# Performance work log

Hardware: AMD Instinct MI355X
Metric: run time of the kernel (lower is better)

The kernel has to match this reference:

```python
import jax, jax.numpy as jnp
import numpy as np

ALPHA = 0.2          # LeakyReLU negative slope
BN_EPS = 1e-5
NEG_INF = -9e15


def setup_inputs() -> dict:
    key = jax.random.key(0)
    k1, k2, k3, k4 = jax.random.split(key, 4)
    B, N, Fin, Fout = 4, 4096, 64, 64
    h = jax.random.normal(k1, (B, N, Fin), dtype=jnp.float32)
    adj = jax.random.randint(k2, (N, N), 0, 2, dtype=jnp.int32)
    # xavier_uniform with gain 1.414
    gain = 1.414
    bW = gain * np.sqrt(6.0 / (Fin + Fout))
    W = jax.random.uniform(k3, (Fin, Fout), dtype=jnp.float32, minval=-bW, maxval=bW)
    ba = gain * np.sqrt(6.0 / (2 * Fout + 1))
    a = jax.random.uniform(k4, (2 * Fout, 1), dtype=jnp.float32, minval=-ba, maxval=ba)
    gamma = jnp.ones((N,), dtype=jnp.float32)
    beta = jnp.zeros((N,), dtype=jnp.float32)
    return {"h": h, "adj": adj, "W": W, "a": a, "gamma": gamma, "beta": beta}


def reference(h, adj, W, a, gamma, beta):
    # h: [B,N,Fin], adj: [N,N], W: [Fin,Fout], a: [2*Fout,1]
    N = adj.shape[0]
    Fout = W.shape[1]
    dk = jnp.asarray(N, h.dtype) ** 0.5
    Wh = jnp.einsum('bnf,fo->bno', h, W)                # [B,N,Fout]
    Wh1 = Wh @ a[:Fout]                                 # [B,N,1]
    Wh2 = Wh @ a[Fout:]                                 # [B,N,1]
    e = (Wh1 + jnp.swapaxes(Wh2, 1, 2)) / dk            # [B,N,N] broadcast add
    e = jax.nn.leaky_relu(e, negative_slope=ALPHA)
    scores = jnp.where(adj[None] > 0, e, NEG_INF)
    attention = jax.nn.softmax(scores, axis=2)          # dropout is identity at inference
    h_prime = jnp.einsum('bij,bjo->bio', attention, Wh) # [B,N,Fout]
    # BatchNorm1d(N): channel axis is the node axis, normalize over (B, Fout)
    mean = h_prime.mean(axis=(0, 2), keepdims=True)
    var = h_prime.var(axis=(0, 2), keepdims=True)
    h_prime = gamma[None, :, None] * (h_prime - mean) * jax.lax.rsqrt(var + BN_EPS) + beta[None, :, None]
    out = h_prime + h                                   # in==out -> res_net is None
    return jax.nn.elu(out)                              # concat=True
```

## Files before the change

### kernel.cpp

```cpp
#include <hip/hip_runtime.h>
#include <hip/hip_fp16.h>
#include <math.h>

#define NN 4096
#define SCL 0.022542110013890054f
#define LOG2E 1.4426950408889634f

typedef __attribute__((ext_vector_type(8))) _Float16 f16x8;
typedef __attribute__((ext_vector_type(2))) _Float16 f16x2;
typedef __attribute__((ext_vector_type(4))) float f32x4;
typedef __attribute__((ext_vector_type(4))) short s16x4;

__device__ __forceinline__ float exp2_fast(float x) {
  float r; asm("v_exp_f32 %0, %1" : "=v"(r) : "v"(x)); return r;
}
__device__ __forceinline__ unsigned short h16(float x) {
  _Float16 h = (_Float16)x; return *(unsigned short*)&h;
}

__global__ __launch_bounds__(256)
void k_prep(const float* __restrict__ h, const float* __restrict__ W,
            const float* __restrict__ a, const int* __restrict__ adj,
            unsigned short* __restrict__ WhTf, unsigned* __restrict__ Ei1,
            unsigned* __restrict__ Ei2, unsigned* __restrict__ Ej1,
            unsigned* __restrict__ Ej2, unsigned* __restrict__ bits) {
  __shared__ float sW[4096];
  __shared__ unsigned short T[64][8];
  const int t = threadIdx.x;
  const int bi = blockIdx.x;
  const int r3 = bi % 3, q3 = bi / 3;
  if (r3 == 0) {
    const int w = t >> 6, lane = t & 63;
    const int r = q3 * 4 + w;
    const int kq = lane >> 1, hi = lane & 1;
#pragma unroll
    for (int half = 0; half < 2; ++half) {
      const int* __restrict__ src = adj + ((size_t)r << 12) + half * 2048;
      int v[32];
#pragma unroll
      for (int k = 0; k < 32; ++k) v[k] = src[k * 64 + lane];
      unsigned myw = 0;
#pragma unroll
      for (int k = 0; k < 32; ++k) {
        unsigned long long m = __ballot(v[k] != 0);
        unsigned lohi = hi ? (unsigned)(m >> 32) : (unsigned)m;
        myw = (kq == k) ? lohi : myw;
      }
      bits[((size_t)r << 7) + half * 64 + lane] = myw;
    }
    return;
  }
#pragma unroll
  for (int i = 0; i < 16; ++i) sW[i * 256 + t] = W[i * 256 + t];
  __syncthreads();
  const int wv = t >> 6, lane = t & 63;
  const float a1 = a[lane], a2 = a[64 + lane];
  const int row0 = (q3 * 2 + (r3 - 1)) * 8;
  const int q0 = row0 + wv * 2;
  float w1v[2], w2v[2];
  for (int r = 0; r < 2; ++r) {
    const int row = q0 + r;
    const float* hr = h + (size_t)row * 64;
    float acc = 0.f;
#pragma unroll
    for (int k = 0; k < 64; ++k) acc = fmaf(hr[k], sW[k * 64 + lane], acc);
    T[lane][wv * 2 + r] = h16(acc);
    float r1 = acc * a1, r2 = acc * a2;
#pragma unroll
    for (int sft = 32; sft; sft >>= 1) { r1 += __shfl_xor(r1, sft); r2 += __shfl_xor(r2, sft); }
    w1v[r] = r1 * SCL; w2v[r] = r2 * SCL;
  }
  if (lane == 0) {
#pragma unroll
    for (int r = 0; r < 2; ++r) {
      unsigned u1 = h16(exp2_fast(w1v[r]));
      unsigned u2 = h16(exp2_fast(0.2f * w1v[r]));
      Ei1[q0 + r] = u1 | (u1 << 16);
      Ei2[q0 + r] = u2 | (u2 << 16);
    }
    Ej1[q0 >> 1] = (unsigned)h16(exp2_fast(w2v[0])) |
                   ((unsigned)h16(exp2_fast(w2v[1])) << 16);
    Ej2[q0 >> 1] = (unsigned)h16(exp2_fast(0.2f * w2v[0])) |
                   ((unsigned)h16(exp2_fast(0.2f * w2v[1])) << 16);
  }
  __syncthreads();
  const int f = t >> 2, jp4 = t & 3;
  const int b = row0 >> 12, n0 = row0 & 4095;
  const int g32 = n0 >> 5, rgq = (n0 >> 3) & 3;
  unsigned v = *(unsigned*)&T[f][jp4 * 2];
  unsigned short* dst = WhTf +
      ((((size_t)(b * 4 + (f >> 4)) << 7) + g32) << 9) +
      ((rgq * 16 + (f & 15)) << 3) + jp4 * 2;
  *(unsigned*)dst = v;
}

__global__ __launch_bounds__(512, 2)
void k_gat(const unsigned* __restrict__ bits,
           const unsigned short* __restrict__ WhTf,
           const unsigned* __restrict__ Ei1, const unsigned* __restrict__ Ei2,
           const unsigned* __restrict__ Ej1, const unsigned* __restrict__ Ej2,
           unsigned short* __restrict__ Pp, float* __restrict__ lsp) {
  __shared__ unsigned mlds[256][17];

  const int t = threadIdx.x;
  const int w = t >> 6, lane = t & 63;
  const int jp = lane & 15, rg = lane >> 4;
  const int bid = blockIdx.x;
  const int c = bid >> 6;
  const int b = (bid >> 4) & 3;
  const int i0b = (bid & 15) * 256;
  const int i0 = i0b + w * 32;
  const int g0 = c * 16;

#pragma unroll
  for (int pass = 0; pass < 8; ++pass) {
    const int row = pass * 32 + (t >> 4);
    mlds[row][t & 15] = bits[((size_t)(i0b + row) << 7) + g0 + (t & 15)];
  }

  unsigned ei1u[2], ei2u[2];
#pragma unroll
  for (int il = 0; il < 2; ++il) {
    ei1u[il] = Ei1[b * NN + i0 + il * 16 + jp];
    ei2u[il] = Ei2[b * NN + i0 + il * 16 + jp];
  }
  const unsigned short* __restrict__ abase =
      WhTf + (((size_t)(b * 4) << 7) + g0) * 512 + lane * 8;
  const unsigned* __restrict__ ej1b = Ej1 + (b << 11) + (g0 << 4) + (rg << 2);
  const unsigned* __restrict__ ej2b = Ej2 + (b << 11) + (g0 << 4) + (rg << 2);

  f32x4 acc[2][4];
  f32x4 accd[2];
#pragma unroll
  for (int il = 0; il < 2; ++il) {
    accd[il] = (f32x4){0.f, 0.f, 0.f, 0.f};
#pragma unroll
    for (int ft = 0; ft < 4; ++ft) acc[il][ft] = (f32x4){0.f, 0.f, 0.f, 0.f};
  }
  f16x8 ones;
#pragma unroll
  for (int e = 0; e < 8; ++e) ones[e] = (_Float16)1.0f;

  __syncthreads();

#pragma unroll 2
  for (int jt = 0; jt < 16; ++jt) {
    const f16x8 af0 = *(const f16x8*)(abase + (0 * 128 + jt) * 512);
    const f16x8 af1 = *(const f16x8*)(abase + (1 * 128 + jt) * 512);
    const f16x8 af2 = *(const f16x8*)(abase + (2 * 128 + jt) * 512);
    const f16x8 af3 = *(const f16x8*)(abase + (3 * 128 + jt) * 512);
    const uint4 e1p = *(const uint4*)(ej1b + jt * 16);
    const uint4 e2p = *(const uint4*)(ej2b + jt * 16);
    const unsigned e1a[4] = {e1p.x, e1p.y, e1p.z, e1p.w};
    const unsigned e2a[4] = {e2p.x, e2p.y, e2p.z, e2p.w};

    f16x8 pf[2];
#pragma unroll
    for (int il = 0; il < 2; ++il) {
      const unsigned mb = mlds[w * 32 + il * 16 + jp][jt] >> (rg * 8);
      const f16x2 x1 = *(const f16x2*)&ei1u[il];
      const f16x2 x2 = *(const f16x2*)&ei2u[il];
      unsigned pw[4];
#pragma unroll
      for (int p4 = 0; p4 < 4; ++p4) {
        f16x2 c1 = x1 * (*(const f16x2*)&e1a[p4]);
        f16x2 c2 = x2 * (*(const f16x2*)&e2a[p4]);
        f16x2 mx = __builtin_elementwise_max(c1, c2);
        unsigned mexp = (((mb >> (2 * p4)) & 1u) ? 0xFFFFu : 0u) |
                        (((mb >> (2 * p4 + 1)) & 1u) ? 0xFFFF0000u : 0u);
        pw[p4] = (*(unsigned*)&mx) & mexp;
      }
      pf[il] = *(f16x8*)pw;
    }
#pragma unroll
    for (int il = 0; il < 2; ++il) {
      accd[il] = __builtin_amdgcn_mfma_f32_16x16x32_f16(ones, pf[il], accd[il], 0, 0, 0);
      acc[il][0] = __builtin_amdgcn_mfma_f32_16x16x32_f16(af0, pf[il], acc[il][0], 0, 0, 0);
      acc[il][1] = __builtin_amdgcn_mfma_f32_16x16x32_f16(af1, pf[il], acc[il][1], 0, 0, 0);
      acc[il][2] = __builtin_amdgcn_mfma_f32_16x16x32_f16(af2, pf[il], acc[il][2], 0, 0, 0);
      acc[il][3] = __builtin_amdgcn_mfma_f32_16x16x32_f16(af3, pf[il], acc[il][3], 0, 0, 0);
    }
  }

  if (rg == 0) {
#pragma unroll
    for (int il = 0; il < 2; ++il)
      lsp[(size_t)(c * 4 + b) * NN + i0 + il * 16 + jp] = accd[il][0];
  }
  const size_t pbase = (((size_t)(c * 4 + b)) * NN + i0) * 64;
#pragma unroll
  for (int il = 0; il < 2; ++il)
#pragma unroll
    for (int ft = 0; ft < 4; ++ft) {
      s16x4 pk;
#pragma unroll
      for (int r = 0; r < 4; ++r) pk[r] = (short)h16(acc[il][ft][r]);
      *(s16x4*)(Pp + pbase + (size_t)(il * 16 + jp) * 64 + ft * 16 + rg * 4) = pk;
    }
}

__global__ __launch_bounds__(256)
void k_bn(const float* __restrict__ h, const unsigned short* __restrict__ Pp,
          const float* __restrict__ lsp, const float* __restrict__ gamma,
          const float* __restrict__ beta, float* __restrict__ out) {
  __shared__ float bnp[2][4][2];
  const int t = threadIdx.x;
  const int w = t >> 6, lane = t & 63;
  const int i0 = blockIdx.x * 2;
  float x[2];
#pragma unroll
  for (int ii = 0; ii < 2; ++ii) {
    const int i = i0 + ii;
    float xv = 0.f, lt = 0.f;
#pragma unroll
    for (int cc = 0; cc < 8; ++cc) {
      xv += (float)(*(const _Float16*)(Pp + ((size_t)(cc * 4 + w) * NN + i) * 64 + lane));
      lt += lsp[(size_t)(cc * 4 + w) * NN + i];
    }
    xv /= lt;
    x[ii] = xv;
    float s1 = xv, s2 = xv * xv;
#pragma unroll
    for (int m = 32; m; m >>= 1) { s1 += __shfl_xor(s1, m); s2 += __shfl_xor(s2, m); }
    if (lane == 0) { bnp[ii][w][0] = s1; bnp[ii][w][1] = s2; }
  }
  __syncthreads();
#pragma unroll
  for (int ii = 0; ii < 2; ++ii) {
    const float t1 = bnp[ii][0][0] + bnp[ii][1][0] + bnp[ii][2][0] + bnp[ii][3][0];
    const float t2 = bnp[ii][0][1] + bnp[ii][1][1] + bnp[ii][2][1] + bnp[ii][3][1];
    const float mean = t1 * (1.f / 256.f);
    const float var  = t2 * (1.f / 256.f) - mean * mean;
    const float sc = gamma[i0 + ii] * rsqrtf(var + 1e-5f);
    const float bt = beta[i0 + ii];
    const size_t off = (((size_t)(w * NN + i0 + ii)) << 6) + lane;
    float o = sc * (x[ii] - mean) + bt + h[off];
    o = o > 0.f ? o : exp2_fast(o * LOG2E) - 1.f;
    out[off] = o;
  }
}

extern "C" void kernel_launch(void* const* d_in, const int* in_sizes, int n_in,
                              void* d_out, int out_size, void* d_ws, size_t ws_size,
                              hipStream_t stream) {
  (void)in_sizes; (void)n_in; (void)out_size; (void)ws_size;
  const float* h     = (const float*)d_in[0];
  const int*   adj   = (const int*)d_in[1];
  const float* W     = (const float*)d_in[2];
  const float* a     = (const float*)d_in[3];
  const float* gamma = (const float*)d_in[4];
  const float* beta  = (const float*)d_in[5];
  float* out = (float*)d_out;

  char* ws = (char*)d_ws;
  unsigned short* WhTf = (unsigned short*)ws;
  unsigned* bits = (unsigned*)(ws + (2u << 20));
  unsigned* Ei1 = (unsigned*)(ws + (4u << 20));
  unsigned* Ei2 = (unsigned*)(ws + (4u << 20) + (64u << 10));
  unsigned* Ej1 = (unsigned*)(ws + (4u << 20) + (128u << 10));
  unsigned* Ej2 = (unsigned*)(ws + (4u << 20) + (160u << 10));
  float* lsp = (float*)(ws + (4u << 20) + (192u << 10));
  unsigned short* Pp = (unsigned short*)(ws + (5u << 20));

  k_prep<<<3072, 256, 0, stream>>>(h, W, a, adj, WhTf, Ei1, Ei2, Ej1, Ej2, bits);
  k_gat<<<512, 512, 0, stream>>>(bits, WhTf, Ei1, Ei2, Ej1, Ej2, Pp, lsp);
  k_bn<<<2048, 256, 0, stream>>>(h, Pp, lsp, gamma, beta, out);
}
```

Before: 51.39 us.

## Read int32 adjacency directly in attention kernel instead of prepacked bitmask

Removes the adjacency bit-packing stage from the prep kernel and the LDS staging of the bitmask in the attention kernel. Each lane now loads its int32 adjacency entries straight from global memory inside the j-loop and builds the f16 mask from them. This saves a kernel phase and a barrier. In exchange the attention kernel reads the full 64MB int32 adjacency, and each of the 4 batch blocks rereads it rather than sharing a 2MB bitmask, so memory traffic rises sharply.

```diff
diff --git a/kernel.cpp b/kernel.cpp
--- a/kernel.cpp
+++ b/kernel.cpp
@@ -20,42 +20,19 @@
 
 __global__ __launch_bounds__(256)
 void k_prep(const float* __restrict__ h, const float* __restrict__ W,
-            const float* __restrict__ a, const int* __restrict__ adj,
-            unsigned short* __restrict__ WhTf, unsigned* __restrict__ Ei1,
-            unsigned* __restrict__ Ei2, unsigned* __restrict__ Ej1,
-            unsigned* __restrict__ Ej2, unsigned* __restrict__ bits) {
+            const float* __restrict__ a, unsigned short* __restrict__ WhTf,
+            unsigned* __restrict__ Ei1, unsigned* __restrict__ Ei2,
+            unsigned* __restrict__ Ej1, unsigned* __restrict__ Ej2) {
   __shared__ float sW[4096];
   __shared__ unsigned short T[64][8];
   const int t = threadIdx.x;
   const int bi = blockIdx.x;
-  const int r3 = bi % 3, q3 = bi / 3;
-  if (r3 == 0) {
-    const int w = t >> 6, lane = t & 63;
-    const int r = q3 * 4 + w;
-    const int kq = lane >> 1, hi = lane & 1;
-#pragma unroll
-    for (int half = 0; half < 2; ++half) {
-      const int* __restrict__ src = adj + ((size_t)r << 12) + half * 2048;
-      int v[32];
-#pragma unroll
-      for (int k = 0; k < 32; ++k) v[k] = src[k * 64 + lane];
-      unsigned myw = 0;
-#pragma unroll
-      for (int k = 0; k < 32; ++k) {
-        unsigned long long m = __ballot(v[k] != 0);
-        unsigned lohi = hi ? (unsigned)(m >> 32) : (unsigned)m;
-        myw = (kq == k) ? lohi : myw;
-      }
-      bits[((size_t)r << 7) + half * 64 + lane] = myw;
-    }
-    return;
-  }
 #pragma unroll
   for (int i = 0; i < 16; ++i) sW[i * 256 + t] = W[i * 256 + t];
   __syncthreads();
   const int wv = t >> 6, lane = t & 63;
   const float a1 = a[lane], a2 = a[64 + lane];
-  const int row0 = (q3 * 2 + (r3 - 1)) * 8;
+  const int row0 = bi * 8;
   const int q0 = row0 + wv * 2;
   float w1v[2], w2v[2];
   for (int r = 0; r < 2; ++r) {
@@ -95,13 +72,11 @@
 }
 
 __global__ __launch_bounds__(512, 2)
-void k_gat(const unsigned* __restrict__ bits,
+void k_gat(const int* __restrict__ adj,
            const unsigned short* __restrict__ WhTf,
            const unsigned* __restrict__ Ei1, const unsigned* __restrict__ Ei2,
            const unsigned* __restrict__ Ej1, const unsigned* __restrict__ Ej2,
            unsigned short* __restrict__ Pp, float* __restrict__ lsp) {
-  __shared__ unsigned mlds[256][17];
-
   const int t = threadIdx.x;
   const int w = t >> 6, lane = t & 63;
   const int jp = lane & 15, rg = lane >> 4;
@@ -112,18 +87,14 @@
   const int i0 = i0b + w * 32;
   const int g0 = c * 16;
 
-#pragma unroll
-  for (int pass = 0; pass < 8; ++pass) {
-    const int row = pass * 32 + (t >> 4);
-    mlds[row][t & 15] = bits[((size_t)(i0b + row) << 7) + g0 + (t & 15)];
-  }
-
   unsigned ei1u[2], ei2u[2];
 #pragma unroll
   for (int il = 0; il < 2; ++il) {
     ei1u[il] = Ei1[b * NN + i0 + il * 16 + jp];
     ei2u[il] = Ei2[b * NN + i0 + il * 16 + jp];
   }
+  const int* __restrict__ arow0 = adj + (((size_t)(i0 + jp)) << 12) + g0 * 32 + rg * 8;
+  const int* __restrict__ arow1 = arow0 + ((size_t)16 << 12);
   const unsigned short* __restrict__ abase =
       WhTf + (((size_t)(b * 4) << 7) + g0) * 512 + lane * 8;
   const unsigned* __restrict__ ej1b = Ej1 + (b << 11) + (g0 << 4) + (rg << 2);
@@ -140,8 +111,6 @@
   f16x8 ones;
 #pragma unroll
   for (int e = 0; e < 8; ++e) ones[e] = (_Float16)1.0f;
-
-  __syncthreads();
 
 #pragma unroll 2
   for (int jt = 0; jt < 16; ++jt) {
@@ -151,13 +120,19 @@
     const f16x8 af3 = *(const f16x8*)(abase + (3 * 128 + jt) * 512);
     const uint4 e1p = *(const uint4*)(ej1b + jt * 16);
     const uint4 e2p = *(const uint4*)(ej2b + jt * 16);
+    const int4 ma0 = *(const int4*)(arow0 + jt * 32);
+    const int4 mb0 = *(const int4*)(arow0 + jt * 32 + 4);
+    const int4 ma1 = *(const int4*)(arow1 + jt * 32);
+    const int4 mb1 = *(const int4*)(arow1 + jt * 32 + 4);
     const unsigned e1a[4] = {e1p.x, e1p.y, e1p.z, e1p.w};
     const unsigned e2a[4] = {e2p.x, e2p.y, e2p.z, e2p.w};
+    const int av[2][8] = {
+        {ma0.x, ma0.y, ma0.z, ma0.w, mb0.x, mb0.y, mb0.z, mb0.w},
+        {ma1.x, ma1.y, ma1.z, ma1.w, mb1.x, mb1.y, mb1.z, mb1.w}};
 
     f16x8 pf[2];
 #pragma unroll
     for (int il = 0; il < 2; ++il) {
-      const unsigned mb = mlds[w * 32 + il * 16 + jp][jt] >> (rg * 8);
       const f16x2 x1 = *(const f16x2*)&ei1u[il];
       const f16x2 x2 = *(const f16x2*)&ei2u[il];
       unsigned pw[4];
@@ -166,8 +141,8 @@
         f16x2 c1 = x1 * (*(const f16x2*)&e1a[p4]);
         f16x2 c2 = x2 * (*(const f16x2*)&e2a[p4]);
         f16x2 mx = __builtin_elementwise_max(c1, c2);
-        unsigned mexp = (((mb >> (2 * p4)) & 1u) ? 0xFFFFu : 0u) |
-                        (((mb >> (2 * p4 + 1)) & 1u) ? 0xFFFF0000u : 0u);
+        unsigned mexp = (av[il][2 * p4] ? 0xFFFFu : 0u) |
+                        (av[il][2 * p4 + 1] ? 0xFFFF0000u : 0u);
         pw[p4] = (*(unsigned*)&mx) & mexp;
       }
       pf[il] = *(f16x8*)pw;
@@ -254,7 +229,6 @@
 
   char* ws = (char*)d_ws;
   unsigned short* WhTf = (unsigned short*)ws;
-  unsigned* bits = (unsigned*)(ws + (2u << 20));
   unsigned* Ei1 = (unsigned*)(ws + (4u << 20));
   unsigned* Ei2 = (unsigned*)(ws + (4u << 20) + (64u << 10));
   unsigned* Ej1 = (unsigned*)(ws + (4u << 20) + (128u << 10));
@@ -262,7 +236,7 @@
   float* lsp = (float*)(ws + (4u << 20) + (192u << 10));
   unsigned short* Pp = (unsigned short*)(ws + (5u << 20));
 
-  k_prep<<<3072, 256, 0, stream>>>(h, W, a, adj, WhTf, Ei1, Ei2, Ej1, Ej2, bits);
-  k_gat<<<512, 512, 0, stream>>>(bits, WhTf, Ei1, Ei2, Ej1, Ej2, Pp, lsp);
+  k_prep<<<2048, 256, 0, stream>>>(h, W, a, WhTf, Ei1, Ei2, Ej1, Ej2);
+  k_gat<<<512, 512, 0, stream>>>(adj, WhTf, Ei1, Ei2, Ej1, Ej2, Pp, lsp);
   k_bn<<<2048, 256, 0, stream>>>(h, Pp, lsp, gamma, beta, out);
 }
```

Result: slower. 68.66 us (+33.6%).
